# Kernel optimization log

Hardware: AMD Instinct MI355X
Metric: run time of the kernel (lower is better)

Reference implementation:

```python
import jax, jax.numpy as jnp
import numpy as np
from jax import lax

B, NK, NQ, DK, DV, H = 4, 4096, 4096, 64, 64, 256


def _linear_params(key, fan_in, fan_out):
    kw, kb = jax.random.split(key)
    lim = 1.0 / np.sqrt(fan_in)
    w = jax.random.uniform(kw, (fan_out, fan_in), jnp.float32, -lim, lim)
    b = jax.random.uniform(kb, (fan_out,), jnp.float32, -lim, lim)
    return w, b


def setup_inputs() -> dict:
    key = jax.random.key(0)
    ks = jax.random.split(key, 9)
    inp = {
        "KEY": jax.random.normal(ks[0], (B, NK, DK), jnp.float32),
        "VALUE": jax.random.normal(ks[1], (B, NK, DV), jnp.float32),
        "QUERY": jax.random.normal(ks[2], (B, NQ, DK), jnp.float32),
    }
    inp["W1_w"], inp["W1_b"] = _linear_params(ks[3], DK, H)
    inp["W2_w"], inp["W2_b"] = _linear_params(ks[4], H, H)
    inp["W3_w"], inp["W3_b"] = _linear_params(ks[5], H, DK)
    inp["Wo1_w"], inp["Wo1_b"] = _linear_params(ks[6], DK, H)
    inp["Wo2_w"], inp["Wo2_b"] = _linear_params(ks[7], H, H)
    inp["Wo3_w"], inp["Wo3_b"] = _linear_params(ks[8], H, DV)
    return inp


def _mlp(x, w1, b1, w2, b2, w3, b3):
    h = jax.nn.relu(jnp.einsum('bnd,hd->bnh', x, w1) + b1)
    h = jax.nn.relu(jnp.einsum('bnh,gh->bng', h, w2) + b2)
    return jnp.einsum('bng,og->bno', h, w3) + b3


def _l1_cdist(K, Q):
    # K: [b,nk,d], Q: [b,nq,d] -> [b,nk,nq]; scan over feature dim to avoid
    # materializing the [b,nk,nq,d] difference tensor.
    b, nk, _ = K.shape
    nq = Q.shape[1]

    def body(acc, kq):
        k, q = kq  # [b,nk], [b,nq]
        return acc + jnp.abs(k[:, :, None] - q[:, None, :]), None

    init = jnp.zeros((b, nk, nq), K.dtype)
    score, _ = lax.scan(body, init, (jnp.moveaxis(K, -1, 0), jnp.moveaxis(Q, -1, 0)))
    return score


def reference(KEY, VALUE, QUERY, W1_w, W1_b, W2_w, W2_b, W3_w, W3_b,
              Wo1_w, Wo1_b, Wo2_w, Wo2_b, Wo3_w, Wo3_b):
    Wk = _mlp(KEY, W1_w, W1_b, W2_w, W2_b, W3_w, W3_b)
    Wq = _mlp(QUERY, W1_w, W1_b, W2_w, W2_b, W3_w, W3_b)
    Wo = _mlp(QUERY, Wo1_w, Wo1_b, Wo2_w, Wo2_b, Wo3_w, Wo3_b)
    KEY_scale = KEY * Wk          # [b,nk,dk]
    QUERY_scale = QUERY * Wq      # [b,nq,dk]
    score = _l1_cdist(KEY_scale, QUERY_scale)            # [b,nk,nq]
    attn = jax.nn.softmax(-(score * score) * 0.5, axis=1)  # softmax over keys
    context = jnp.einsum('bik,bij->bkj', attn, VALUE)    # [b,nq,dv]
    # dropout is identity in eval mode
    return context * Wo
```

## Files before the change

### kernel.cpp

```cpp
#include <hip/hip_runtime.h>
#include <hip/hip_bf16.h>
#include <stdint.h>

#define B_DIM 4
#define NKK 4096
#define NQQ 4096
#define DD 64
#define HH 256

typedef __attribute__((ext_vector_type(4))) float floatx4;
typedef __attribute__((ext_vector_type(2))) float floatx2;
typedef __attribute__((ext_vector_type(8))) short bf16x8;

__device__ __forceinline__ float fexp2(float x) { return __builtin_amdgcn_exp2f(x); }
__device__ __forceinline__ unsigned fbits(float x) { return __float_as_uint(x); }
__device__ __forceinline__ float bf2f(unsigned short u) { return __uint_as_float(((unsigned)u) << 16); }

__device__ __forceinline__ floatx2 pk_sub(floatx2 a, floatx2 b) {
  floatx2 d;
  asm("v_pk_add_f32 %0, %1, %2 neg_lo:[0,1] neg_hi:[0,1]" : "=v"(d) : "v"(a), "v"(b));
  return d;
}

__device__ __forceinline__ void splitbf(float x, unsigned short& h, unsigned short& l) {
  unsigned u = fbits(x);
  unsigned hu = (u + 0x7fff + ((u >> 16) & 1)) & 0xffff0000u;
  h = (unsigned short)(hu >> 16);
  l = (unsigned short)(fbits(x - __uint_as_float(hu)) >> 16);
}

#define FSTRIDE 68
#define FSTRIDE4 17

__global__ __launch_bounds__(256) void wsplit_kernel(
    const float* __restrict__ W1a, const float* __restrict__ W2a, const float* __restrict__ W3a,
    const float* __restrict__ W1b, const float* __restrict__ W2b, const float* __restrict__ W3b,
    unsigned short* __restrict__ sp)
{
  int idx = blockIdx.x * 256 + threadIdx.x;
  const int set = idx >= 98304;
  int r = idx - set * 98304;
  unsigned short* base = sp + (size_t)set * 196608;
  const float* src;
  unsigned short *dh, *dl;
  int j;
  if (r < 16384)      { src = set ? W1b : W1a; dh = base;          dl = base + 16384;  j = r; }
  else if (r < 81920) { src = set ? W2b : W2a; dh = base + 32768;  dl = base + 98304;  j = r - 16384; }
  else                { src = set ? W3b : W3a; dh = base + 163840; dl = base + 180224; j = r - 81920; }
  unsigned short h, l;
  splitbf(src[j], h, l);
  dh[j] = h; dl[j] = l;
}

__global__ __launch_bounds__(256) void vtrans_kernel(
    const float* __restrict__ V, unsigned short* __restrict__ Vt)
{
  __shared__ unsigned short t[64][80];
  const int tid = threadIdx.x;
  const int b = blockIdx.y;
  const int k0 = blockIdx.x * 64;
  const float4* V4 = (const float4*)V;
  {
    const int r = tid & 63;
    const int c4 = tid >> 6;
#pragma unroll
    for (int j = 0; j < 4; ++j) {
      float4 f = V4[((size_t)(b * NKK + k0 + r)) * 16 + c4 * 4 + j];
      const int d0 = c4 * 16 + j * 4;
      t[d0 + 0][r] = (unsigned short)(fbits(f.x) >> 16);
      t[d0 + 1][r] = (unsigned short)(fbits(f.y) >> 16);
      t[d0 + 2][r] = (unsigned short)(fbits(f.z) >> 16);
      t[d0 + 3][r] = (unsigned short)(fbits(f.w) >> 16);
    }
  }
  __syncthreads();
  {
    const int d = tid >> 2;
    const int kc = tid & 3;
    uint4 u0 = *(const uint4*)&t[d][kc * 16];
    uint4 u1 = *(const uint4*)&t[d][kc * 16 + 8];
    unsigned short* dst = Vt + ((size_t)(b * 64 + d)) * NKK + k0 + kc * 16;
    *(uint4*)dst = u0;
    *(uint4*)(dst + 8) = u1;
  }
}

#define HSTRIDE 264
__global__ __launch_bounds__(512, 1) void mlpmm_kernel(
    const float* __restrict__ KEY, const float* __restrict__ QUERY,
    const float* __restrict__ B1a, const float* __restrict__ B2a, const float* __restrict__ B3a,
    const float* __restrict__ B1b, const float* __restrict__ B2b, const float* __restrict__ B3b,
    const unsigned short* __restrict__ sp,
    float* __restrict__ Ks, float* __restrict__ Qs, float* __restrict__ Wo)
{
  __shared__ unsigned short Xh[64][72], Xl[64][72];
  __shared__ unsigned short Hsh[64][HSTRIDE], Hsl[64][HSTRIDE];
  const int tid = threadIdx.x;
  const int w = tid >> 6;
  const int lane = tid & 63;
  const int l15 = lane & 15;
  const int quad = lane >> 4;

  const int g = blockIdx.x;
  const float* X;
  float* outp;
  int mulx, t0;
  const unsigned short* wb;
  const float *b1, *b2, *b3;
  if (g < 256)      { X = KEY;   outp = Ks; mulx = 1; t0 = g * 64;         wb = sp;          b1 = B1a; b2 = B2a; b3 = B3a; }
  else if (g < 512) { X = QUERY; outp = Qs; mulx = 1; t0 = (g - 256) * 64; wb = sp;          b1 = B1a; b2 = B2a; b3 = B3a; }
  else              { X = QUERY; outp = Wo; mulx = 0; t0 = (g - 512) * 64; wb = sp + 196608; b1 = B1b; b2 = B2b; b3 = B3b; }
  const unsigned short* W1h = wb;
  const unsigned short* W1l = wb + 16384;
  const unsigned short* W2h = wb + 32768;
  const unsigned short* W2l = wb + 98304;
  const unsigned short* W3h = wb + 163840;
  const unsigned short* W3l = wb + 180224;

  {
    const int t = tid >> 3;
    const int c = (tid & 7) * 8;
    float4 a = *(const float4*)&X[(size_t)(t0 + t) * 64 + c];
    float4 b = *(const float4*)&X[(size_t)(t0 + t) * 64 + c + 4];
    float v[8] = {a.x, a.y, a.z, a.w, b.x, b.y, b.z, b.w};
    unsigned short hs[8], ls[8];
#pragma unroll
    for (int e = 0; e < 8; ++e) splitbf(v[e], hs[e], ls[e]);
    uint4 uh = make_uint4(hs[0] | ((unsigned)hs[1] << 16), hs[2] | ((unsigned)hs[3] << 16),
                          hs[4] | ((unsigned)hs[5] << 16), hs[6] | ((unsigned)hs[7] << 16));
    uint4 ul = make_uint4(ls[0] | ((unsigned)ls[1] << 16), ls[2] | ((unsigned)ls[3] << 16),
                          ls[4] | ((unsigned)ls[5] << 16), ls[6] | ((unsigned)ls[7] << 16));
    *(uint4*)&Xh[t][c] = uh;
    *(uint4*)&Xl[t][c] = ul;
  }
  __syncthreads();

  {
    floatx4 acc[4][2];
#pragma unroll
    for (int nb = 0; nb < 2; ++nb) {
      const float bias = b1[(w * 2 + nb) * 16 + l15];
#pragma unroll
      for (int mb = 0; mb < 4; ++mb) acc[mb][nb] = (floatx4){bias, bias, bias, bias};
    }
#pragma unroll
    for (int kb = 0; kb < 2; ++kb) {
      bf16x8 Ah[4], Al[4];
#pragma unroll
      for (int mb = 0; mb < 4; ++mb) {
        Ah[mb] = *(const bf16x8*)&Xh[mb * 16 + l15][kb * 32 + quad * 8];
        Al[mb] = *(const bf16x8*)&Xl[mb * 16 + l15][kb * 32 + quad * 8];
      }
#pragma unroll
      for (int nb = 0; nb < 2; ++nb) {
        const int n0 = (w * 2 + nb) * 16;
        bf16x8 Bh = *(const bf16x8*)&W1h[(size_t)(n0 + l15) * 64 + kb * 32 + quad * 8];
        bf16x8 Bl = *(const bf16x8*)&W1l[(size_t)(n0 + l15) * 64 + kb * 32 + quad * 8];
#pragma unroll
        for (int mb = 0; mb < 4; ++mb) {
          acc[mb][nb] = __builtin_amdgcn_mfma_f32_16x16x32_bf16(Ah[mb], Bh, acc[mb][nb], 0, 0, 0);
          acc[mb][nb] = __builtin_amdgcn_mfma_f32_16x16x32_bf16(Al[mb], Bh, acc[mb][nb], 0, 0, 0);
          acc[mb][nb] = __builtin_amdgcn_mfma_f32_16x16x32_bf16(Ah[mb], Bl, acc[mb][nb], 0, 0, 0);
        }
      }
    }
#pragma unroll
    for (int mb = 0; mb < 4; ++mb)
#pragma unroll
      for (int nb = 0; nb < 2; ++nb) {
        const int col = (w * 2 + nb) * 16 + l15;
#pragma unroll
        for (int r = 0; r < 4; ++r) {
          const int row = mb * 16 + quad * 4 + r;
          float v = fmaxf(acc[mb][nb][r], 0.0f);
          unsigned short h, l;
          splitbf(v, h, l);
          Hsh[row][col] = h;
          Hsl[row][col] = l;
        }
      }
  }
  __syncthreads();

  {
    floatx4 acc2[4][2];
#pragma unroll
    for (int nb = 0; nb < 2; ++nb) {
      const float bias = b2[(w * 2 + nb) * 16 + l15];
#pragma unroll
      for (int mb = 0; mb < 4; ++mb) acc2[mb][nb] = (floatx4){bias, bias, bias, bias};
    }
#pragma unroll
    for (int kb = 0; kb < 8; ++kb) {
      bf16x8 Ah[4], Al[4];
#pragma unroll
      for (int mb = 0; mb < 4; ++mb) {
        Ah[mb] = *(const bf16x8*)&Hsh[mb * 16 + l15][kb * 32 + quad * 8];
        Al[mb] = *(const bf16x8*)&Hsl[mb * 16 + l15][kb * 32 + quad * 8];
      }
#pragma unroll
      for (int nb = 0; nb < 2; ++nb) {
        const int n0 = (w * 2 + nb) * 16;
        bf16x8 Bh = *(const bf16x8*)&W2h[(size_t)(n0 + l15) * 256 + kb * 32 + quad * 8];
        bf16x8 Bl = *(const bf16x8*)&W2l[(size_t)(n0 + l15) * 256 + kb * 32 + quad * 8];
#pragma unroll
        for (int mb = 0; mb < 4; ++mb) {
          acc2[mb][nb] = __builtin_amdgcn_mfma_f32_16x16x32_bf16(Ah[mb], Bh, acc2[mb][nb], 0, 0, 0);
          acc2[mb][nb] = __builtin_amdgcn_mfma_f32_16x16x32_bf16(Al[mb], Bh, acc2[mb][nb], 0, 0, 0);
          acc2[mb][nb] = __builtin_amdgcn_mfma_f32_16x16x32_bf16(Ah[mb], Bl, acc2[mb][nb], 0, 0, 0);
        }
      }
    }
    __syncthreads();
#pragma unroll
    for (int mb = 0; mb < 4; ++mb)
#pragma unroll
      for (int nb = 0; nb < 2; ++nb) {
        const int col = (w * 2 + nb) * 16 + l15;
#pragma unroll
        for (int r = 0; r < 4; ++r) {
          const int row = mb * 16 + quad * 4 + r;
          float v = fmaxf(acc2[mb][nb][r], 0.0f);
          unsigned short h, l;
          splitbf(v, h, l);
          Hsh[row][col] = h;
          Hsl[row][col] = l;
        }
      }
  }
  __syncthreads();

  {
    const int mp = (w >> 2) * 2;
    const int n0 = (w & 3) * 16;
    const float bias = b3[n0 + l15];
    floatx4 acc3[2];
#pragma unroll
    for (int m = 0; m < 2; ++m) acc3[m] = (floatx4){bias, bias, bias, bias};
#pragma unroll
    for (int kb = 0; kb < 8; ++kb) {
      bf16x8 Ah[2], Al[2];
#pragma unroll
      for (int m = 0; m < 2; ++m) {
        Ah[m] = *(const bf16x8*)&Hsh[(mp + m) * 16 + l15][kb * 32 + quad * 8];
        Al[m] = *(const bf16x8*)&Hsl[(mp + m) * 16 + l15][kb * 32 + quad * 8];
      }
      bf16x8 Bh = *(const bf16x8*)&W3h[(size_t)(n0 + l15) * 256 + kb * 32 + quad * 8];
      bf16x8 Bl = *(const bf16x8*)&W3l[(size_t)(n0 + l15) * 256 + kb * 32 + quad * 8];
#pragma unroll
      for (int m = 0; m < 2; ++m) {
        acc3[m] = __builtin_amdgcn_mfma_f32_16x16x32_bf16(Ah[m], Bh, acc3[m], 0, 0, 0);
        acc3[m] = __builtin_amdgcn_mfma_f32_16x16x32_bf16(Al[m], Bh, acc3[m], 0, 0, 0);
        acc3[m] = __builtin_amdgcn_mfma_f32_16x16x32_bf16(Ah[m], Bl, acc3[m], 0, 0, 0);
      }
    }
#pragma unroll
    for (int m = 0; m < 2; ++m)
#pragma unroll
      for (int r = 0; r < 4; ++r) {
        const int row = (mp + m) * 16 + quad * 4 + r;
        const int col = n0 + l15;
        float v = acc3[m][r];
        if (mulx) v *= (bf2f(Xh[row][col]) + bf2f(Xl[row][col]));
        outp[(size_t)(t0 + row) * 64 + col] = v;
      }
  }
}

__global__ __launch_bounds__(256, 2) void attn_kernel(
    const float* __restrict__ Ksg, const float* __restrict__ Qsg,
    const unsigned short* __restrict__ Vtg, const float* __restrict__ Wog,
    float* __restrict__ outp)
{
  __shared__ float qsA[32 * FSTRIDE];
  __shared__ float ksA[4][32 * FSTRIDE];
  __shared__ unsigned short vtB[4][64 * 40];
  __shared__ unsigned short psB[4][32 * 40];
  __shared__ float abA[4][32];
  __shared__ float mbufA[4][32];
  __shared__ float lbufA[4][32];

  const int tid  = threadIdx.x;
  const int w    = tid >> 6;
  const int lane = tid & 63;
  const int lq   = lane >> 3;
  const int lk   = lane & 7;
  const int l15  = lane & 15;
  const int quad = lane >> 4;
  const int b    = blockIdx.y;
  const int qt   = blockIdx.x * 32;

  {
    const int row = tid >> 3;
    const int c0  = (tid & 7) * 2;
    const float4* Q4 = (const float4*)Qsg;
    float4 g0 = Q4[(size_t)(b * NQQ + qt + row) * 16 + c0];
    float4 g1 = Q4[(size_t)(b * NQQ + qt + row) * 16 + c0 + 1];
    *(float4*)&qsA[row * FSTRIDE + c0 * 4]     = g0;
    *(float4*)&qsA[row * FSTRIDE + c0 * 4 + 4] = g1;
  }
  __syncthreads();

  float m_i[4], l_i[4];
  floatx4 acc[2][4];
#pragma unroll
  for (int i = 0; i < 4; ++i) { m_i[i] = -3.0e38f; l_i[i] = 0.0f; }
#pragma unroll
  for (int mb = 0; mb < 2; ++mb)
#pragma unroll
    for (int nb = 0; nb < 4; ++nb)
#pragma unroll
      for (int r = 0; r < 4; ++r) acc[mb][nb][r] = 0.0f;

  const int kstart = w * (NKK / 4);
  const float4* K4 = (const float4*)Ksg;
  const unsigned short* vg = Vtg + ((size_t)b * 64 + lane) * NKK + kstart;
  const float NEG_HALF_LOG2E = -0.72134752044448170f;

  const int krow = (lane >> 4);
  const int kci  = lane & 15;
  const int vst  = (lane >> 3) & 3;

  float4 kpre[8];
  uint4 vtpre[4];
#pragma unroll
  for (int c = 0; c < 8; ++c)
    kpre[c] = K4[(size_t)(b * NKK + kstart + c * 4 + krow) * 16 + kci];
#pragma unroll
  for (int c = 0; c < 4; ++c)
    vtpre[c] = *(const uint4*)(vg + c * 8);

  const floatx4* qb = (const floatx4*)&qsA[lq * FSTRIDE];
  const floatx4* kb = (const floatx4*)&ksA[w][lk * FSTRIDE];

  int vcol[4];
#pragma unroll
  for (int nb = 0; nb < 4; ++nb)
    vcol[nb] = (((quad + (l15 >> 3) + 2 * nb) & 3) << 3);

  for (int it = 0; it < (NKK / 4) / 32; ++it) {
#pragma unroll
    for (int c = 0; c < 8; ++c)
      *(float4*)&ksA[w][(c * 4 + krow) * FSTRIDE + kci * 4] = kpre[c];
#pragma unroll
    for (int c = 0; c < 4; ++c)
      *(uint4*)&vtB[w][lane * 40 + (((c + vst) & 3) << 3)] = vtpre[c];

    {
      const int itn = (it + 1 < 32) ? it + 1 : it;
#pragma unroll
      for (int c = 0; c < 8; ++c)
        kpre[c] = K4[(size_t)(b * NKK + kstart + itn * 32 + c * 4 + krow) * 16 + kci];
#pragma unroll
      for (int c = 0; c < 4; ++c)
        vtpre[c] = *(const uint4*)(vg + itn * 32 + c * 8);
    }

    float s[4][4];
#pragma unroll
    for (int i = 0; i < 4; ++i)
#pragma unroll
      for (int j = 0; j < 4; ++j) s[i][j] = 0.0f;

#pragma unroll
    for (int dc = 0; dc < 16; ++dc) {
      floatx4 qv[4], kv[4];
#pragma unroll
      for (int i = 0; i < 4; ++i) qv[i] = qb[i * (8 * FSTRIDE4) + dc];
#pragma unroll
      for (int j = 0; j < 4; ++j) kv[j] = kb[j * (8 * FSTRIDE4) + dc];
#pragma unroll
      for (int i = 0; i < 4; ++i) {
        const floatx2 qlo = qv[i].lo, qhi = qv[i].hi;
#pragma unroll
        for (int j = 0; j < 4; ++j) {
          floatx2 d0 = pk_sub(qlo, kv[j].lo);
          floatx2 d1 = pk_sub(qhi, kv[j].hi);
          s[i][j] += __builtin_fabsf(d0.x);
          s[i][j] += __builtin_fabsf(d0.y);
          s[i][j] += __builtin_fabsf(d1.x);
          s[i][j] += __builtin_fabsf(d1.y);
        }
      }
    }

    float a_row[4];
#pragma unroll
    for (int i = 0; i < 4; ++i) {
      float smin = fminf(fminf(s[i][0], s[i][1]), fminf(s[i][2], s[i][3]));
      smin = fminf(smin, __shfl_xor(smin, 1));
      smin = fminf(smin, __shfl_xor(smin, 2));
      smin = fminf(smin, __shfl_xor(smin, 4));
      const float tmax = smin * smin * NEG_HALF_LOG2E;
      const float mn = fmaxf(m_i[i], tmax);
      a_row[i] = fexp2(m_i[i] - mn);
      m_i[i] = mn;
      float ps = 0.0f;
#pragma unroll
      for (int j = 0; j < 4; ++j) {
        const float sv = s[i][j];
        const float e = fexp2(fmaf(sv * NEG_HALF_LOG2E, sv, -mn));
        ps += e;
        psB[w][(lq + 8 * i) * 40 + lk + 8 * j] = (unsigned short)(fbits(e) >> 16);
      }
      l_i[i] = fmaf(l_i[i], a_row[i], ps);
    }
    if (lk == 0) {
#pragma unroll
      for (int i = 0; i < 4; ++i) abA[w][lq + 8 * i] = a_row[i];
    }

    {
      bf16x8 afrag[2], bfrag[4];
#pragma unroll
      for (int mb = 0; mb < 2; ++mb)
        afrag[mb] = *(const bf16x8*)&psB[w][(mb * 16 + l15) * 40 + quad * 8];
#pragma unroll
      for (int nb = 0; nb < 4; ++nb)
        bfrag[nb] = *(const bf16x8*)&vtB[w][(nb * 16 + l15) * 40 + vcol[nb]];

      const floatx4 arv0 = *(const floatx4*)&abA[w][quad * 4];
      const floatx4 arv1 = *(const floatx4*)&abA[w][16 + quad * 4];

#pragma unroll
      for (int nb = 0; nb < 4; ++nb) {
        acc[0][nb] *= arv0;
        acc[1][nb] *= arv1;
        acc[0][nb] = __builtin_amdgcn_mfma_f32_16x16x32_bf16(afrag[0], bfrag[nb], acc[0][nb], 0, 0, 0);
        acc[1][nb] = __builtin_amdgcn_mfma_f32_16x16x32_bf16(afrag[1], bfrag[nb], acc[1][nb], 0, 0, 0);
      }
    }
  }

#pragma unroll
  for (int i = 0; i < 4; ++i) {
    float l = l_i[i];
    l += __shfl_xor(l, 1);
    l += __shfl_xor(l, 2);
    l += __shfl_xor(l, 4);
    l_i[i] = l;
  }
  if (lk == 0) {
#pragma unroll
    for (int i = 0; i < 4; ++i) {
      mbufA[w][lq + 8 * i] = m_i[i];
      lbufA[w][lq + 8 * i] = l_i[i];
    }
  }
#pragma unroll
  for (int mb = 0; mb < 2; ++mb)
#pragma unroll
    for (int nb = 0; nb < 4; ++nb)
#pragma unroll
      for (int r = 0; r < 4; ++r)
        ksA[w][(mb * 16 + quad * 4 + r) * 64 + nb * 16 + l15] = acc[mb][nb][r];
  __syncthreads();

  {
    const int q = tid >> 3;
    const int dbase = (tid & 7) * 8;
    const float m0 = mbufA[0][q], m1 = mbufA[1][q], m2 = mbufA[2][q], m3 = mbufA[3][q];
    const float M = fmaxf(fmaxf(m0, m1), fmaxf(m2, m3));
    const float s0 = fexp2(m0 - M), s1 = fexp2(m1 - M);
    const float s2v = fexp2(m2 - M), s3 = fexp2(m3 - M);
    const float L = lbufA[0][q] * s0 + lbufA[1][q] * s1 + lbufA[2][q] * s2v + lbufA[3][q] * s3;
    const float rL = 1.0f / L;
    const size_t gbase = (size_t)(b * NQQ + qt + q) * 64 + dbase;
#pragma unroll
    for (int c = 0; c < 8; ++c) {
      const int d = dbase + c;
      float o = s0 * ksA[0][q * 64 + d] + s1 * ksA[1][q * 64 + d] +
                s2v * ksA[2][q * 64 + d] + s3 * ksA[3][q * 64 + d];
      outp[gbase + c] = o * rL * Wog[gbase + c];
    }
  }
}

extern "C" void kernel_launch(void* const* d_in, const int* in_sizes, int n_in,
                              void* d_out, int out_size, void* d_ws, size_t ws_size,
                              hipStream_t stream) {
  (void)in_sizes; (void)n_in; (void)out_size; (void)ws_size;
  const float* KEY   = (const float*)d_in[0];
  const float* VALUE = (const float*)d_in[1];
  const float* QUERY = (const float*)d_in[2];
  const float* W1w = (const float*)d_in[3];
  const float* W1b = (const float*)d_in[4];
  const float* W2w = (const float*)d_in[5];
  const float* W2b = (const float*)d_in[6];
  const float* W3w = (const float*)d_in[7];
  const float* W3b = (const float*)d_in[8];
  const float* Wo1w = (const float*)d_in[9];
  const float* Wo1b = (const float*)d_in[10];
  const float* Wo2w = (const float*)d_in[11];
  const float* Wo2b = (const float*)d_in[12];
  const float* Wo3w = (const float*)d_in[13];
  const float* Wo3b = (const float*)d_in[14];

  float* ws = (float*)d_ws;
  const size_t tsz = (size_t)B_DIM * NKK * DD;
  float* Ks = ws;
  float* Qs = ws + tsz;
  float* Wo = ws + 2 * tsz;
  unsigned short* Vtg = (unsigned short*)(ws + 3 * tsz);
  unsigned short* sp  = Vtg + tsz;
  float* outf = (float*)d_out;

  wsplit_kernel<<<dim3(768), 256, 0, stream>>>(W1w, W2w, W3w, Wo1w, Wo2w, Wo3w, sp);
  vtrans_kernel<<<dim3(NKK / 64, B_DIM), 256, 0, stream>>>(VALUE, Vtg);
  mlpmm_kernel<<<dim3(768), 512, 0, stream>>>(
      KEY, QUERY, W1b, W2b, W3b, Wo1b, Wo2b, Wo3b, sp, Ks, Qs, Wo);
  attn_kernel<<<dim3(NQQ / 32, B_DIM), 256, 0, stream>>>(Ks, Qs, Vtg, Wo, outf);
}
```

Baseline: 433.6 us.

## Split attention over key halves, load V fragments directly, add merge kernel

```diff
diff --git a/kernel.cpp b/kernel.cpp
--- a/kernel.cpp
+++ b/kernel.cpp
@@ -267,18 +267,17 @@
   }
 }
 
-__global__ __launch_bounds__(256, 2) void attn_kernel(
+template <int ITERS, bool PARTIAL>
+__global__ __launch_bounds__(256, 3) void attn_kernel(
     const float* __restrict__ Ksg, const float* __restrict__ Qsg,
     const unsigned short* __restrict__ Vtg, const float* __restrict__ Wog,
-    float* __restrict__ outp)
+    float* __restrict__ outp,
+    float* __restrict__ Pm, float* __restrict__ Pl, float* __restrict__ PO)
 {
   __shared__ float qsA[32 * FSTRIDE];
   __shared__ float ksA[4][32 * FSTRIDE];
-  __shared__ unsigned short vtB[4][64 * 40];
   __shared__ unsigned short psB[4][32 * 40];
   __shared__ float abA[4][32];
-  __shared__ float mbufA[4][32];
-  __shared__ float lbufA[4][32];
 
   const int tid  = threadIdx.x;
   const int w    = tid >> 6;
@@ -312,14 +311,14 @@
 #pragma unroll
       for (int r = 0; r < 4; ++r) acc[mb][nb][r] = 0.0f;
 
-  const int kstart = w * (NKK / 4);
+  const int kstart = (blockIdx.z * 4 + w) * (ITERS * 32);
   const float4* K4 = (const float4*)Ksg;
-  const unsigned short* vg = Vtg + ((size_t)b * 64 + lane) * NKK + kstart;
   const float NEG_HALF_LOG2E = -0.72134752044448170f;
 
   const int krow = (lane >> 4);
   const int kci  = lane & 15;
-  const int vst  = (lane >> 3) & 3;
+
+  const unsigned short* vg0 = Vtg + ((size_t)b * 64 + l15) * NKK + kstart + quad * 8;
 
   float4 kpre[8];
   uint4 vtpre[4];
@@ -327,33 +326,22 @@
   for (int c = 0; c < 8; ++c)
     kpre[c] = K4[(size_t)(b * NKK + kstart + c * 4 + krow) * 16 + kci];
 #pragma unroll
-  for (int c = 0; c < 4; ++c)
-    vtpre[c] = *(const uint4*)(vg + c * 8);
+  for (int nb = 0; nb < 4; ++nb)
+    vtpre[nb] = *(const uint4*)(vg0 + (size_t)nb * 16 * NKK);
 
   const floatx4* qb = (const floatx4*)&qsA[lq * FSTRIDE];
   const floatx4* kb = (const floatx4*)&ksA[w][lk * FSTRIDE];
 
-  int vcol[4];
-#pragma unroll
-  for (int nb = 0; nb < 4; ++nb)
-    vcol[nb] = (((quad + (l15 >> 3) + 2 * nb) & 3) << 3);
-
-  for (int it = 0; it < (NKK / 4) / 32; ++it) {
+  for (int it = 0; it < ITERS; ++it) {
 #pragma unroll
     for (int c = 0; c < 8; ++c)
       *(float4*)&ksA[w][(c * 4 + krow) * FSTRIDE + kci * 4] = kpre[c];
-#pragma unroll
-    for (int c = 0; c < 4; ++c)
-      *(uint4*)&vtB[w][lane * 40 + (((c + vst) & 3) << 3)] = vtpre[c];
 
     {
-      const int itn = (it + 1 < 32) ? it + 1 : it;
+      const int itn = (it + 1 < ITERS) ? it + 1 : it;
 #pragma unroll
       for (int c = 0; c < 8; ++c)
         kpre[c] = K4[(size_t)(b * NKK + kstart + itn * 32 + c * 4 + krow) * 16 + kci];
-#pragma unroll
-      for (int c = 0; c < 4; ++c)
-        vtpre[c] = *(const uint4*)(vg + itn * 32 + c * 8);
     }
 
     float s[4][4];
@@ -411,24 +399,29 @@
     }
 
     {
-      bf16x8 afrag[2], bfrag[4];
+      bf16x8 afrag[2];
 #pragma unroll
       for (int mb = 0; mb < 2; ++mb)
         afrag[mb] = *(const bf16x8*)&psB[w][(mb * 16 + l15) * 40 + quad * 8];
-#pragma unroll
-      for (int nb = 0; nb < 4; ++nb)
-        bfrag[nb] = *(const bf16x8*)&vtB[w][(nb * 16 + l15) * 40 + vcol[nb]];
 
       const floatx4 arv0 = *(const floatx4*)&abA[w][quad * 4];
       const floatx4 arv1 = *(const floatx4*)&abA[w][16 + quad * 4];
 
 #pragma unroll
       for (int nb = 0; nb < 4; ++nb) {
+        bf16x8 bfrag = __builtin_bit_cast(bf16x8, vtpre[nb]);
         acc[0][nb] *= arv0;
         acc[1][nb] *= arv1;
-        acc[0][nb] = __builtin_amdgcn_mfma_f32_16x16x32_bf16(afrag[0], bfrag[nb], acc[0][nb], 0, 0, 0);
-        acc[1][nb] = __builtin_amdgcn_mfma_f32_16x16x32_bf16(afrag[1], bfrag[nb], acc[1][nb], 0, 0, 0);
-      }
+        acc[0][nb] = __builtin_amdgcn_mfma_f32_16x16x32_bf16(afrag[0], bfrag, acc[0][nb], 0, 0, 0);
+        acc[1][nb] = __builtin_amdgcn_mfma_f32_16x16x32_bf16(afrag[1], bfrag, acc[1][nb], 0, 0, 0);
+      }
+    }
+
+    {
+      const int itn = (it + 1 < ITERS) ? it + 1 : it;
+#pragma unroll
+      for (int nb = 0; nb < 4; ++nb)
+        vtpre[nb] = *(const uint4*)(vg0 + (size_t)nb * 16 * NKK + itn * 32);
     }
   }
 
@@ -440,11 +433,12 @@
     l += __shfl_xor(l, 4);
     l_i[i] = l;
   }
+  float* ovl = (float*)&psB[w][0];
   if (lk == 0) {
 #pragma unroll
     for (int i = 0; i < 4; ++i) {
-      mbufA[w][lq + 8 * i] = m_i[i];
-      lbufA[w][lq + 8 * i] = l_i[i];
+      ovl[lq + 8 * i]      = m_i[i];
+      ovl[32 + lq + 8 * i] = l_i[i];
     }
   }
 #pragma unroll
@@ -459,27 +453,70 @@
   {
     const int q = tid >> 3;
     const int dbase = (tid & 7) * 8;
-    const float m0 = mbufA[0][q], m1 = mbufA[1][q], m2 = mbufA[2][q], m3 = mbufA[3][q];
+    const float m0 = ((const float*)&psB[0][0])[q];
+    const float m1 = ((const float*)&psB[1][0])[q];
+    const float m2 = ((const float*)&psB[2][0])[q];
+    const float m3 = ((const float*)&psB[3][0])[q];
     const float M = fmaxf(fmaxf(m0, m1), fmaxf(m2, m3));
     const float s0 = fexp2(m0 - M), s1 = fexp2(m1 - M);
     const float s2v = fexp2(m2 - M), s3 = fexp2(m3 - M);
-    const float L = lbufA[0][q] * s0 + lbufA[1][q] * s1 + lbufA[2][q] * s2v + lbufA[3][q] * s3;
-    const float rL = 1.0f / L;
-    const size_t gbase = (size_t)(b * NQQ + qt + q) * 64 + dbase;
-#pragma unroll
-    for (int c = 0; c < 8; ++c) {
-      const int d = dbase + c;
-      float o = s0 * ksA[0][q * 64 + d] + s1 * ksA[1][q * 64 + d] +
-                s2v * ksA[2][q * 64 + d] + s3 * ksA[3][q * 64 + d];
-      outp[gbase + c] = o * rL * Wog[gbase + c];
-    }
-  }
+    const float L = ((const float*)&psB[0][0])[32 + q] * s0 +
+                    ((const float*)&psB[1][0])[32 + q] * s1 +
+                    ((const float*)&psB[2][0])[32 + q] * s2v +
+                    ((const float*)&psB[3][0])[32 + q] * s3;
+    if (PARTIAL) {
+      const size_t p = (size_t)(blockIdx.z * 4 + b) * 128 + blockIdx.x;
+      if (dbase == 0) { Pm[p * 32 + q] = M; Pl[p * 32 + q] = L; }
+      float* dst = PO + p * 2048 + q * 64 + dbase;
+#pragma unroll
+      for (int c = 0; c < 8; ++c) {
+        const int d = dbase + c;
+        dst[c] = s0 * ksA[0][q * 64 + d] + s1 * ksA[1][q * 64 + d] +
+                 s2v * ksA[2][q * 64 + d] + s3 * ksA[3][q * 64 + d];
+      }
+    } else {
+      const float rL = 1.0f / L;
+      const size_t gbase = (size_t)(b * NQQ + qt + q) * 64 + dbase;
+#pragma unroll
+      for (int c = 0; c < 8; ++c) {
+        const int d = dbase + c;
+        float o = s0 * ksA[0][q * 64 + d] + s1 * ksA[1][q * 64 + d] +
+                  s2v * ksA[2][q * 64 + d] + s3 * ksA[3][q * 64 + d];
+        outp[gbase + c] = o * rL * Wog[gbase + c];
+      }
+    }
+  }
+}
+
+__global__ __launch_bounds__(256) void amerge_kernel(
+    const float* __restrict__ Pm, const float* __restrict__ Pl,
+    const float* __restrict__ PO, const float* __restrict__ Wog,
+    float* __restrict__ outp)
+{
+  const int tid = threadIdx.x;
+  const int qt = blockIdx.x;
+  const int b = blockIdx.y;
+  const int q = tid >> 3;
+  const int dbase = (tid & 7) * 8;
+  const size_t p0 = (size_t)b * 128 + qt;
+  const size_t p1 = (size_t)(4 + b) * 128 + qt;
+  const float m0 = Pm[p0 * 32 + q], m1 = Pm[p1 * 32 + q];
+  const float l0 = Pl[p0 * 32 + q], l1 = Pl[p1 * 32 + q];
+  const float M = fmaxf(m0, m1);
+  const float w0 = fexp2(m0 - M), w1 = fexp2(m1 - M);
+  const float rL = 1.0f / (w0 * l0 + w1 * l1);
+  const float* o0 = PO + p0 * 2048 + q * 64 + dbase;
+  const float* o1 = PO + p1 * 2048 + q * 64 + dbase;
+  const size_t g = ((size_t)b * NQQ + qt * 32 + q) * 64 + dbase;
+#pragma unroll
+  for (int c = 0; c < 8; ++c)
+    outp[g + c] = (w0 * o0[c] + w1 * o1[c]) * rL * Wog[g + c];
 }
 
 extern "C" void kernel_launch(void* const* d_in, const int* in_sizes, int n_in,
                               void* d_out, int out_size, void* d_ws, size_t ws_size,
                               hipStream_t stream) {
-  (void)in_sizes; (void)n_in; (void)out_size; (void)ws_size;
+  (void)in_sizes; (void)n_in; (void)out_size;
   const float* KEY   = (const float*)d_in[0];
   const float* VALUE = (const float*)d_in[1];
   const float* QUERY = (const float*)d_in[2];
@@ -503,11 +540,24 @@
   float* Wo = ws + 2 * tsz;
   unsigned short* Vtg = (unsigned short*)(ws + 3 * tsz);
   unsigned short* sp  = Vtg + tsz;
+  float* Pm = ws + 3 * tsz + tsz / 2 + 196608;
+  float* Pl = Pm + 32768;
+  float* PO = Pl + 32768;
   float* outf = (float*)d_out;
+
+  const size_t ws_need = (size_t)(3 * tsz + tsz / 2 + 196608 + 2 * 32768 + 2097152) * 4;
+  const bool partial = ws_size >= ws_need;
 
   wsplit_kernel<<<dim3(768), 256, 0, stream>>>(W1w, W2w, W3w, Wo1w, Wo2w, Wo3w, sp);
   vtrans_kernel<<<dim3(NKK / 64, B_DIM), 256, 0, stream>>>(VALUE, Vtg);
   mlpmm_kernel<<<dim3(768), 512, 0, stream>>>(
       KEY, QUERY, W1b, W2b, W3b, Wo1b, Wo2b, Wo3b, sp, Ks, Qs, Wo);
-  attn_kernel<<<dim3(NQQ / 32, B_DIM), 256, 0, stream>>>(Ks, Qs, Vtg, Wo, outf);
-}
+  if (partial) {
+    attn_kernel<16, true><<<dim3(NQQ / 32, B_DIM, 2), 256, 0, stream>>>(
+        Ks, Qs, Vtg, Wo, outf, Pm, Pl, PO);
+    amerge_kernel<<<dim3(NQQ / 32, B_DIM), 256, 0, stream>>>(Pm, Pl, PO, Wo, outf);
+  } else {
+    attn_kernel<32, false><<<dim3(NQQ / 32, B_DIM, 1), 256, 0, stream>>>(
+        Ks, Qs, Vtg, Wo, outf, Pm, Pl, PO);
+  }
+}
```

Measured after the change: 440.5 us. No clear change (+1.6%).
